# Optimization experiments

Measured on AMD Instinct MI355X. Metric: run time of the kernel, lower is better.

The kernel has to match this reference:

```python
import jax, jax.numpy as jnp
import numpy as np

N_NODES = 100000
N_EDGES = 3200000
N_FEAT = 128
DIM = 64
N_GRAPHS = 4096
EPS = 1e-5


def setup_inputs() -> dict:
    key = jax.random.key(0)
    ks = jax.random.split(key, 20)
    x = jax.random.normal(ks[0], (N_NODES, N_FEAT), dtype=jnp.float32)
    edge_index = jax.random.randint(ks[1], (2, N_EDGES), 0, N_NODES, dtype=jnp.int64)
    batch = jnp.sort(jax.random.randint(ks[2], (N_NODES,), 0, N_GRAPHS, dtype=jnp.int64))
    s = 0.1
    inp = {
        "x": x, "edge_index": edge_index, "batch": batch,
        "w1": jax.random.normal(ks[3], (N_FEAT, DIM), jnp.float32) * s,
        "b1": jnp.zeros((DIM,), jnp.float32),
        "bn1_g": 1.0 + s * jax.random.normal(ks[4], (DIM,), jnp.float32),
        "bn1_b": s * jax.random.normal(ks[5], (DIM,), jnp.float32),
        "conv_w": jax.random.normal(ks[6], (3, DIM, DIM), jnp.float32) * s,
        "conv_b": jnp.zeros((3, DIM), jnp.float32),
        "bnc_g": 1.0 + s * jax.random.normal(ks[7], (3, DIM), jnp.float32),
        "bnc_b": s * jax.random.normal(ks[8], (3, DIM), jnp.float32),
        "mlp_w": jax.random.normal(ks[9], (3, DIM, DIM), jnp.float32) * s,
        "mlp_b": jnp.zeros((3, DIM), jnp.float32),
        "bnm_g": 1.0 + s * jax.random.normal(ks[10], (3, DIM), jnp.float32),
        "bnm_b": s * jax.random.normal(ks[11], (3, DIM), jnp.float32),
        "out_w": jax.random.normal(ks[12], (DIM, 1), jnp.float32) * s,
        "out_b": jnp.zeros((1,), jnp.float32),
    }
    return inp


def _batchnorm(h, g, b):
    # training-mode BN: batch stats over the node/graph axis, biased variance
    m = jnp.mean(h, axis=0)
    v = jnp.var(h, axis=0)
    return (h - m) * jax.lax.rsqrt(v + EPS) * g + b


def _forward(x, edge_index, batch, w1, b1, bn1_g, bn1_b, conv_w, conv_b,
             bnc_g, bnc_b, mlp_w, mlp_b, bnm_g, bnm_b, out_w, out_b):
    src, dst = edge_index[0], edge_index[1]
    n = x.shape[0]
    # degree with self-loops (GCNConv default: add_self_loops=True, sym norm)
    deg = jax.ops.segment_sum(jnp.ones((src.shape[0],), x.dtype), dst, num_segments=n) + 1.0
    dis = jax.lax.rsqrt(deg)                  # D^{-1/2}
    enorm = (dis[src] * dis[dst])[:, None]    # per-edge norm [E,1]
    self_norm = (dis * dis)[:, None]          # self-loop norm = 1/deg [N,1]

    def gcn(h, W, b):
        h = h @ W                                                  # lin first (PyG)
        agg = jax.ops.segment_sum(h[src] * enorm, dst, num_segments=n)
        return agg + h * self_norm + b

    h = _batchnorm(jax.nn.relu(gcn(x, w1, b1)), bn1_g, bn1_b)
    for i in range(3):
        h = _batchnorm(gcn(h, conv_w[i], conv_b[i]), bnc_g[i], bnc_b[i])
    p = jax.ops.segment_sum(h, batch, num_segments=N_GRAPHS)       # global_add_pool
    for i in range(3):
        p = _batchnorm(jax.nn.relu(p @ mlp_w[i] + mlp_b[i]), bnm_g[i], bnm_b[i])
        # dropout: eval mode -> identity
    return p @ out_w + out_b


def reference(x, edge_index, batch, w1, b1, bn1_g, bn1_b, conv_w, conv_b,
              bnc_g, bnc_b, mlp_w, mlp_b, bnm_g, bnm_b, out_w, out_b):
    return _forward(x, edge_index, batch, w1, b1, bn1_g, bn1_b, conv_w, conv_b,
                    bnc_g, bnc_b, mlp_w, mlp_b, bnm_g, bnm_b, out_w, out_b)
```

## Files before the change

kernel.cpp:

```cpp
#include <hip/hip_runtime.h>
#include <hip/hip_bf16.h>

#define N_FEAT 128
#define DIM 64


__global__ void hist_kernel(const int* __restrict__ dst, int E, int* __restrict__ cnt) {
    int e = blockIdx.x * blockDim.x + threadIdx.x;
    if (e < E) atomicAdd(&cnt[dst[e]], 1);
}

__global__ void dis_kernel(const int* __restrict__ cnt, float* __restrict__ dis, int N) {
    int i = blockIdx.x * blockDim.x + threadIdx.x;
    if (i < N) dis[i] = rsqrtf((float)cnt[i] + 1.0f);
}

__global__ void scanA_kernel(const int* __restrict__ cnt, int N,
                             int* __restrict__ tmp, int* __restrict__ blk) {
    __shared__ int ts[256];
    int t = threadIdx.x;
    int base = blockIdx.x * 1024 + t * 4;
    int v[4];
    int s = 0;
#pragma unroll
    for (int j = 0; j < 4; j++) {
        int i = base + j;
        v[j] = (i < N) ? ((cnt[i] + 7) & ~7) : 0;
        s += v[j];
    }
    ts[t] = s;
    __syncthreads();
    for (int off = 1; off < 256; off <<= 1) {
        int x = (t >= off) ? ts[t - off] : 0;
        __syncthreads();
        ts[t] += x;
        __syncthreads();
    }
    int run = ts[t] - s;
#pragma unroll
    for (int j = 0; j < 4; j++) {
        run += v[j];
        int i = base + j;
        if (i < N) tmp[i] = run;
    }
    if (t == 255) blk[blockIdx.x] = ts[255];
}

__global__ void scanB_kernel(int* __restrict__ blk, int nb) {
    __shared__ int ts[128];
    int t = threadIdx.x;
    int v = (t < nb) ? blk[t] : 0;
    ts[t] = v;
    __syncthreads();
    for (int off = 1; off < 128; off <<= 1) {
        int x = (t >= off) ? ts[t - off] : 0;
        __syncthreads();
        ts[t] += x;
        __syncthreads();
    }
    if (t < nb) blk[t] = ts[t] - v;
}

__global__ void scanC_kernel(const int* __restrict__ tmp, const int* __restrict__ blk,
                             const int* __restrict__ cnt,
                             int N, int* __restrict__ rowp, int* __restrict__ cur) {
    int i = blockIdx.x * blockDim.x + threadIdx.x;
    if (i < N) {
        int b = i >> 10;
        int local = i & 1023;
        int excl = blk[b] + (local ? tmp[i - 1] : 0);
        rowp[i] = excl;
        cur[i] = excl;
        if (i == N - 1) rowp[N] = excl + ((cnt[i] + 7) & ~7);
    }
}

#define NSLICE 256
__global__ __launch_bounds__(256) void fill8_kernel(
    const int* __restrict__ src, const int* __restrict__ dst, int E,
    const float* __restrict__ dis, int* __restrict__ cur,
    int2* __restrict__ ecw, int npx ) {
    int xcd = blockIdx.x & 7;
    int slice = blockIdx.x >> 3;
    int per = (E + NSLICE - 1) / NSLICE;
    int lo = slice * per;
    int hi = min(lo + per, E);
    int dlo = xcd * npx, dhi = dlo + npx;
    for (int e = lo + threadIdx.x; e < hi; e += 256) {
        int d = dst[e];
        if (d >= dlo && d < dhi) {
            int s = src[e];
            int pos = atomicAdd(&cur[d], 1);
            ecw[pos] = make_int2(s << 8, __float_as_int(dis[s] * dis[d]));
        }
    }
}

__global__ void pad_kernel(const int* __restrict__ cur, const int* __restrict__ rowp,
                           int2* __restrict__ ecw, int N) {
    int i = blockIdx.x * blockDim.x + threadIdx.x;
    if (i < N) {
        int p = cur[i], e = rowp[i + 1];
        for (; p < e; p++) ecw[p] = make_int2(0, 0);
    }
}


template<int K, bool AFFINE, bool BIAS, bool RELU, bool STATS>
__global__ __launch_bounds__(256) void gemm_kernel(
    const float* __restrict__ A, const float* __restrict__ W,
    const float* __restrict__ scale, const float* __restrict__ shift,
    const float* __restrict__ bias, float* __restrict__ C,
    float* __restrict__ stats, int M)
{
    __shared__ float As[64][K + 4];
    __shared__ float Ws[K][64];
    __shared__ float bs[64], bq[64];
    int t = threadIdx.x;
    int row0 = blockIdx.x * 64;

    for (int q = t; q < K * 16; q += 256) {
        int k = q >> 4, c4 = (q & 15) << 2;
        float4 w = *reinterpret_cast<const float4*>(&W[k * 64 + c4]);
        *reinterpret_cast<float4*>(&Ws[k][c4]) = w;
    }
    for (int q = t; q < 64 * (K / 4); q += 256) {
        int r = q / (K / 4);
        int k4 = (q % (K / 4)) * 4;
        int row = row0 + r;
        float4 a;
        if (row < M) {
            a = *reinterpret_cast<const float4*>(&A[(size_t)row * K + k4]);
            if (AFFINE) {
                a.x = a.x * scale[k4]     + shift[k4];
                a.y = a.y * scale[k4 + 1] + shift[k4 + 1];
                a.z = a.z * scale[k4 + 2] + shift[k4 + 2];
                a.w = a.w * scale[k4 + 3] + shift[k4 + 3];
            }
        } else {
            a = make_float4(0.f, 0.f, 0.f, 0.f);
        }
        *reinterpret_cast<float4*>(&As[r][k4]) = a;
    }
    __syncthreads();

    int ty = t >> 4, tx = t & 15;
    int r0 = ty * 4, c0 = tx * 4;
    float acc[4][4] = {};
#pragma unroll 2
    for (int k = 0; k < K; k += 4) {
        float4 A0 = *reinterpret_cast<const float4*>(&As[r0 + 0][k]);
        float4 A1 = *reinterpret_cast<const float4*>(&As[r0 + 1][k]);
        float4 A2 = *reinterpret_cast<const float4*>(&As[r0 + 2][k]);
        float4 A3 = *reinterpret_cast<const float4*>(&As[r0 + 3][k]);
        float ar[4][4] = {{A0.x, A0.y, A0.z, A0.w}, {A1.x, A1.y, A1.z, A1.w},
                          {A2.x, A2.y, A2.z, A2.w}, {A3.x, A3.y, A3.z, A3.w}};
#pragma unroll
        for (int kk = 0; kk < 4; kk++) {
            float4 w = *reinterpret_cast<const float4*>(&Ws[k + kk][c0]);
#pragma unroll
            for (int i = 0; i < 4; i++) {
                acc[i][0] += ar[i][kk] * w.x;
                acc[i][1] += ar[i][kk] * w.y;
                acc[i][2] += ar[i][kk] * w.z;
                acc[i][3] += ar[i][kk] * w.w;
            }
        }
    }

    if (STATS) {
        if (t < 64) { bs[t] = 0.f; bq[t] = 0.f; }
        __syncthreads();
    }
    float ssum[4] = {0.f, 0.f, 0.f, 0.f}, ssq[4] = {0.f, 0.f, 0.f, 0.f};
#pragma unroll
    for (int i = 0; i < 4; i++) {
        int row = row0 + r0 + i;
        if (row < M) {
            float4 v;
            float* vp = &v.x;
#pragma unroll
            for (int j = 0; j < 4; j++) {
                float x = acc[i][j];
                if (BIAS) x += bias[c0 + j];
                if (RELU) x = fmaxf(x, 0.f);
                vp[j] = x;
                if (STATS) { ssum[j] += x; ssq[j] += x * x; }
            }
            *reinterpret_cast<float4*>(&C[(size_t)row * 64 + c0]) = v;
        }
    }
    if (STATS) {
#pragma unroll
        for (int j = 0; j < 4; j++) {
            atomicAdd(&bs[c0 + j], ssum[j]);
            atomicAdd(&bq[c0 + j], ssq[j]);
        }
        __syncthreads();
        if (t < 64) {
            atomicAdd(&stats[t], bs[t]);
            atomicAdd(&stats[64 + t], bq[t]);
        }
    }
}


#define LOADP(P, ebase)                                     \
    _Pragma("unroll") for (int j = 0; j < 4; j++)           \
        P[j] = ecw4[((ebase) >> 1) + j];

#define FMAG(P) {                                                          \
    float h[8];                                                            \
    _Pragma("unroll") for (int j = 0; j < 4; j++) {                        \
        h[2*j]   = *(const float*)(Hb + ((unsigned)P[j].x + lane4));       \
        h[2*j+1] = *(const float*)(Hb + ((unsigned)P[j].z + lane4));       \
    }                                                                      \
    _Pragma("unroll") for (int j = 0; j < 4; j++) {                        \
        acc += h[2*j]   * __int_as_float(P[j].y);                          \
        acc += h[2*j+1] * __int_as_float(P[j].w);                          \
    } }

template<bool RELU>
__global__ __launch_bounds__(256) void agg_kernel(
    const float* __restrict__ H, const int* __restrict__ rowp,
    const int2* __restrict__ ecw,
    const float* __restrict__ dis, const float* __restrict__ bias,
    float* __restrict__ Hout, float* __restrict__ stats, int N)
{
    __shared__ float bs[64], bq[64];
    const int4* ecw4 = (const int4*)ecw;
    int t = threadIdx.x;
    int lane = t & 63;
    unsigned lane4 = (unsigned)lane << 2;
    const char* Hb = (const char*)H;
    int base = (blockIdx.x * 4 + (t >> 6)) * 8;
    float b = bias[lane];
    float ssum = 0.f, ssq = 0.f;
    for (int u = 0; u < 8; u++) {
        int n = base + u;
        if (n >= N) break;
        int e0 = rowp[n], e1 = rowp[n + 1];
        float acc = 0.f;
        int ng = (e1 - e0) >> 3;
        if (ng > 0) {
            int4 pa[4], pb[4];
            int e = e0;
            LOADP(pa, e);
            int rem = ng - 1;
            while (rem >= 2) {
                LOADP(pb, e + 8); FMAG(pa);
                LOADP(pa, e + 16); FMAG(pb);
                e += 16; rem -= 2;
            }
            if (rem == 1) { LOADP(pb, e + 8); FMAG(pa); FMAG(pb); }
            else { FMAG(pa); }
        }
        float dn = dis[n];
        acc += H[(size_t)n * 64 + lane] * (dn * dn);
        acc += b;
        if (RELU) acc = fmaxf(acc, 0.f);
        Hout[(size_t)n * 64 + lane] = acc;
        ssum += acc;
        ssq += acc * acc;
    }
    if (t < 64) { bs[t] = 0.f; bq[t] = 0.f; }
    __syncthreads();
    atomicAdd(&bs[lane], ssum);
    atomicAdd(&bq[lane], ssq);
    __syncthreads();
    if (t < 64) {
        atomicAdd(&stats[t], bs[t]);
        atomicAdd(&stats[64 + t], bq[t]);
    }
}


__global__ void bnprep_kernel(const float* __restrict__ stats, const float* __restrict__ g,
                              const float* __restrict__ b, float* __restrict__ ss, float cntInv) {
    int c = threadIdx.x;
    float mean = stats[c] * cntInv;
    float var = stats[64 + c] * cntInv - mean * mean;
    float sc = g[c] * rsqrtf(var + 1e-5f);
    ss[c] = sc;
    ss[64 + c] = b[c] - mean * sc;
}


__global__ __launch_bounds__(256) void pool_kernel(
    const float* __restrict__ H, const int* __restrict__ batch,
    const float* __restrict__ ss, float* __restrict__ P, int N)
{
    int t = threadIdx.x;
    int lane = t & 63;
    int base = (blockIdx.x * 4 + (t >> 6)) * 8;
    float sc = ss[lane], sh = ss[64 + lane];
    float acc = 0.f;
    int gprev = -1;
    for (int u = 0; u < 8; u++) {
        int n = base + u;
        if (n >= N) break;
        int g = batch[n];
        if (g != gprev) {
            if (gprev >= 0) atomicAdd(&P[(size_t)gprev * 64 + lane], acc);
            acc = 0.f;
            gprev = g;
        }
        acc += H[(size_t)n * 64 + lane] * sc + sh;
    }
    if (gprev >= 0) atomicAdd(&P[(size_t)gprev * 64 + lane], acc);
}


__global__ __launch_bounds__(256) void final_kernel(
    const float* __restrict__ P, const float* __restrict__ ss,
    const float* __restrict__ outw, const float* __restrict__ outb,
    float* __restrict__ out, int G)
{
    int t = threadIdx.x;
    int lane = t & 63;
    int g = blockIdx.x * 4 + (t >> 6);
    if (g >= G) return;
    float v = (P[(size_t)g * 64 + lane] * ss[lane] + ss[64 + lane]) * outw[lane];
#pragma unroll
    for (int off = 32; off >= 1; off >>= 1) v += __shfl_xor(v, off, 64);
    if (lane == 0) out[g] = v + outb[0];
}


extern "C" void kernel_launch(void* const* d_in, const int* in_sizes, int n_in,
                              void* d_out, int out_size, void* d_ws, size_t ws_size,
                              hipStream_t stream)
{
    const float* x      = (const float*)d_in[0];
    const int*   ei     = (const int*)d_in[1];
    const int*   batch  = (const int*)d_in[2];
    const float* w1     = (const float*)d_in[3];
    const float* b1     = (const float*)d_in[4];
    const float* bn1_g  = (const float*)d_in[5];
    const float* bn1_b  = (const float*)d_in[6];
    const float* conv_w = (const float*)d_in[7];
    const float* conv_b = (const float*)d_in[8];
    const float* bnc_g  = (const float*)d_in[9];
    const float* bnc_b  = (const float*)d_in[10];
    const float* mlp_w  = (const float*)d_in[11];
    const float* mlp_b  = (const float*)d_in[12];
    const float* bnm_g  = (const float*)d_in[13];
    const float* bnm_b  = (const float*)d_in[14];
    const float* out_w  = (const float*)d_in[15];
    const float* out_b  = (const float*)d_in[16];
    float* out = (float*)d_out;

    const int N = in_sizes[0] / N_FEAT;
    const int E = in_sizes[1] / 2;
    const int G = out_size;
    const int* esrc = ei;
    const int* edst = ei + E;

    char* ws = (char*)d_ws;
    size_t off = 0;
    auto alloc = [&](size_t bytes) {
        size_t cur = off;
        off += (bytes + 255) & ~(size_t)255;
        return (void*)(ws + cur);
    };

    int*   deg   = (int*)alloc((size_t)N * 4);
    float* dis   = (float*)alloc((size_t)N * 4);
    int*   rtmp  = (int*)alloc((size_t)N * 4);
    int*   rowp  = (int*)alloc((size_t)(N + 1) * 4);
    int*   cur   = (int*)alloc((size_t)N * 4);
    int*   blk   = (int*)alloc(256 * 4);
    int2*  ecw   = (int2*)alloc(((size_t)E + 8ull * N) * 8);
    float* bufA  = (float*)alloc((size_t)(N + 64) * 64 * 4);
    float* bufB  = (float*)alloc((size_t)(N + 64) * 64 * 4);
    float* stats = (float*)alloc(7 * 128 * 4);
    float* ssbuf = (float*)alloc(7 * 128 * 4);
    float* P     = (float*)alloc((size_t)G * 64 * 4);
    float* pA    = (float*)alloc((size_t)G * 64 * 4);
    float* pB    = (float*)alloc((size_t)G * 64 * 4);

    hipMemsetAsync(deg, 0, (size_t)N * 4, stream);
    hipMemsetAsync(stats, 0, 7 * 128 * 4, stream);
    hipMemsetAsync(P, 0, (size_t)G * 64 * 4, stream);

    hist_kernel<<<(E + 255) / 256, 256, 0, stream>>>(edst, E, deg);
    dis_kernel<<<(N + 255) / 256, 256, 0, stream>>>(deg, dis, N);
    int nchunk = (N + 1023) / 1024;
    scanA_kernel<<<nchunk, 256, 0, stream>>>(deg, N, rtmp, blk);
    scanB_kernel<<<1, 128, 0, stream>>>(blk, nchunk);
    scanC_kernel<<<(N + 255) / 256, 256, 0, stream>>>(rtmp, blk, deg, N, rowp, cur);
    int npx = (N + 7) / 8;
    fill8_kernel<<<NSLICE * 8, 256, 0, stream>>>(esrc, edst, E, dis, cur, ecw, npx);
    pad_kernel<<<(N + 255) / 256, 256, 0, stream>>>(cur, rowp, ecw, N);

    int gemmN_grid = (N + 63) / 64;
    int aggN_grid = (N + 31) / 32;

    gemm_kernel<128, false, false, false, false><<<gemmN_grid, 256, 0, stream>>>(
        x, w1, nullptr, nullptr, nullptr, bufA, nullptr, N);
    agg_kernel<true><<<aggN_grid, 256, 0, stream>>>(
        bufA, rowp, ecw, dis, b1, bufB, stats, N);
    bnprep_kernel<<<1, 64, 0, stream>>>(stats, bn1_g, bn1_b, ssbuf, 1.0f / N);

    for (int i = 0; i < 3; i++) {
        const float* W  = conv_w + (size_t)i * 64 * 64;
        const float* bb = conv_b + (size_t)i * 64;
        float* st     = stats + (size_t)(1 + i) * 128;
        float* ss_in  = ssbuf + (size_t)i * 128;
        float* ss_out = ssbuf + (size_t)(1 + i) * 128;
        gemm_kernel<64, true, false, false, false><<<gemmN_grid, 256, 0, stream>>>(
            bufB, W, ss_in, ss_in + 64, nullptr, bufA, nullptr, N);
        agg_kernel<false><<<aggN_grid, 256, 0, stream>>>(
            bufA, rowp, ecw, dis, bb, bufB, st, N);
        bnprep_kernel<<<1, 64, 0, stream>>>(st, bnc_g + (size_t)i * 64, bnc_b + (size_t)i * 64,
                                            ss_out, 1.0f / N);
    }

    pool_kernel<<<aggN_grid, 256, 0, stream>>>(bufB, batch, ssbuf + 3 * 128, P, N);

    int gemmG_grid = (G + 63) / 64;
    gemm_kernel<64, false, true, true, true><<<gemmG_grid, 256, 0, stream>>>(
        P, mlp_w, nullptr, nullptr, mlp_b, pA, stats + 4 * 128, G);
    bnprep_kernel<<<1, 64, 0, stream>>>(stats + 4 * 128, bnm_g, bnm_b, ssbuf + 4 * 128, 1.0f / G);

    gemm_kernel<64, true, true, true, true><<<gemmG_grid, 256, 0, stream>>>(
        pA, mlp_w + 64 * 64, ssbuf + 4 * 128, ssbuf + 4 * 128 + 64,
        mlp_b + 64, pB, stats + 5 * 128, G);
    bnprep_kernel<<<1, 64, 0, stream>>>(stats + 5 * 128, bnm_g + 64, bnm_b + 64, ssbuf + 5 * 128, 1.0f / G);

    gemm_kernel<64, true, true, true, true><<<gemmG_grid, 256, 0, stream>>>(
        pB, mlp_w + 2 * 64 * 64, ssbuf + 5 * 128, ssbuf + 5 * 128 + 64,
        mlp_b + 2 * 64, pA, stats + 6 * 128, G);
    bnprep_kernel<<<1, 64, 0, stream>>>(stats + 6 * 128, bnm_g + 2 * 64, bnm_b + 2 * 64, ssbuf + 6 * 128, 1.0f / G);

    final_kernel<<<(G + 3) / 4, 256, 0, stream>>>(pA, ssbuf + 6 * 128, out_w, out_b, out, G);
}
```

Measured before the change: 1.131 ms.

## Factor symmetric GCN norm into GEMM row scaling and shrink edge records

```diff
diff --git a/kernel.cpp b/kernel.cpp
--- a/kernel.cpp
+++ b/kernel.cpp
@@ -7,7 +7,7 @@
 
 __global__ void hist_kernel(const int* __restrict__ dst, int E, int* __restrict__ cnt) {
     int e = blockIdx.x * blockDim.x + threadIdx.x;
-    if (e < E) atomicAdd(&cnt[dst[e]], 1);
+    if (e < E) atomicAdd(&cnt[__builtin_nontemporal_load(&dst[e])], 1);
 }
 
 __global__ void dis_kernel(const int* __restrict__ cnt, float* __restrict__ dis, int N) {
@@ -78,8 +78,7 @@
 #define NSLICE 256
 __global__ __launch_bounds__(256) void fill8_kernel(
     const int* __restrict__ src, const int* __restrict__ dst, int E,
-    const float* __restrict__ dis, int* __restrict__ cur,
-    int2* __restrict__ ecw, int npx ) {
+    int* __restrict__ cur, int* __restrict__ ecwi, int npx) {
     int xcd = blockIdx.x & 7;
     int slice = blockIdx.x >> 3;
     int per = (E + NSLICE - 1) / NSLICE;
@@ -87,31 +86,32 @@
     int hi = min(lo + per, E);
     int dlo = xcd * npx, dhi = dlo + npx;
     for (int e = lo + threadIdx.x; e < hi; e += 256) {
-        int d = dst[e];
+        int d = __builtin_nontemporal_load(&dst[e]);
         if (d >= dlo && d < dhi) {
-            int s = src[e];
+            int s = __builtin_nontemporal_load(&src[e]);
             int pos = atomicAdd(&cur[d], 1);
-            ecw[pos] = make_int2(s << 8, __float_as_int(dis[s] * dis[d]));
+            ecwi[pos] = s << 8;
         }
     }
 }
 
 __global__ void pad_kernel(const int* __restrict__ cur, const int* __restrict__ rowp,
-                           int2* __restrict__ ecw, int N) {
+                           int* __restrict__ ecwi, int N) {
     int i = blockIdx.x * blockDim.x + threadIdx.x;
     if (i < N) {
         int p = cur[i], e = rowp[i + 1];
-        for (; p < e; p++) ecw[p] = make_int2(0, 0);
-    }
-}
-
-
-template<int K, bool AFFINE, bool BIAS, bool RELU, bool STATS>
+        int dummy = N << 8;
+        for (; p < e; p++) ecwi[p] = dummy;
+    }
+}
+
+
+template<int K, bool AFFINE, bool BIAS, bool RELU, bool STATS, bool DISSCALE>
 __global__ __launch_bounds__(256) void gemm_kernel(
     const float* __restrict__ A, const float* __restrict__ W,
     const float* __restrict__ scale, const float* __restrict__ shift,
-    const float* __restrict__ bias, float* __restrict__ C,
-    float* __restrict__ stats, int M)
+    const float* __restrict__ bias, const float* __restrict__ dis,
+    float* __restrict__ C, float* __restrict__ stats, int M)
 {
     __shared__ float As[64][K + 4];
     __shared__ float Ws[K][64];
@@ -177,11 +177,13 @@
     for (int i = 0; i < 4; i++) {
         int row = row0 + r0 + i;
         if (row < M) {
+            float dsc = DISSCALE ? dis[row] : 1.f;
             float4 v;
             float* vp = &v.x;
 #pragma unroll
             for (int j = 0; j < 4; j++) {
                 float x = acc[i][j];
+                if (DISSCALE) x *= dsc;
                 if (BIAS) x += bias[c0 + j];
                 if (RELU) x = fmaxf(x, 0.f);
                 vp[j] = x;
@@ -205,30 +207,27 @@
 }
 
 
-#define LOADP(P, ebase)                                     \
-    _Pragma("unroll") for (int j = 0; j < 4; j++)           \
-        P[j] = ecw4[((ebase) >> 1) + j];
-
-#define FMAG(P) {                                                          \
-    float h[8];                                                            \
-    _Pragma("unroll") for (int j = 0; j < 4; j++) {                        \
-        h[2*j]   = *(const float*)(Hb + ((unsigned)P[j].x + lane4));       \
-        h[2*j+1] = *(const float*)(Hb + ((unsigned)P[j].z + lane4));       \
-    }                                                                      \
-    _Pragma("unroll") for (int j = 0; j < 4; j++) {                        \
-        acc += h[2*j]   * __int_as_float(P[j].y);                          \
-        acc += h[2*j+1] * __int_as_float(P[j].w);                          \
-    } }
+#define SUM8(Q0, Q1) {                                                     \
+    float h0 = *(const float*)(Hb + ((unsigned)Q0.x + lane4));             \
+    float h1 = *(const float*)(Hb + ((unsigned)Q0.y + lane4));             \
+    float h2 = *(const float*)(Hb + ((unsigned)Q0.z + lane4));             \
+    float h3 = *(const float*)(Hb + ((unsigned)Q0.w + lane4));             \
+    float h4 = *(const float*)(Hb + ((unsigned)Q1.x + lane4));             \
+    float h5 = *(const float*)(Hb + ((unsigned)Q1.y + lane4));             \
+    float h6 = *(const float*)(Hb + ((unsigned)Q1.z + lane4));             \
+    float h7 = *(const float*)(Hb + ((unsigned)Q1.w + lane4));             \
+    acc += ((h0 + h1) + (h2 + h3)) + ((h4 + h5) + (h6 + h7));              \
+}
 
 template<bool RELU>
 __global__ __launch_bounds__(256) void agg_kernel(
     const float* __restrict__ H, const int* __restrict__ rowp,
-    const int2* __restrict__ ecw,
+    const int* __restrict__ ecwi,
     const float* __restrict__ dis, const float* __restrict__ bias,
     float* __restrict__ Hout, float* __restrict__ stats, int N)
 {
     __shared__ float bs[64], bq[64];
-    const int4* ecw4 = (const int4*)ecw;
+    const int4* rec4 = (const int4*)ecwi;
     int t = threadIdx.x;
     int lane = t & 63;
     unsigned lane4 = (unsigned)lane << 2;
@@ -243,21 +242,26 @@
         float acc = 0.f;
         int ng = (e1 - e0) >> 3;
         if (ng > 0) {
-            int4 pa[4], pb[4];
-            int e = e0;
-            LOADP(pa, e);
+            int g4 = e0 >> 2;
+            int4 a0 = rec4[g4], a1 = rec4[g4 + 1];
             int rem = ng - 1;
             while (rem >= 2) {
-                LOADP(pb, e + 8); FMAG(pa);
-                LOADP(pa, e + 16); FMAG(pb);
-                e += 16; rem -= 2;
+                int4 b0 = rec4[g4 + 2], b1 = rec4[g4 + 3];
+                SUM8(a0, a1);
+                a0 = rec4[g4 + 4]; a1 = rec4[g4 + 5];
+                SUM8(b0, b1);
+                g4 += 4; rem -= 2;
             }
-            if (rem == 1) { LOADP(pb, e + 8); FMAG(pa); FMAG(pb); }
-            else { FMAG(pa); }
-        }
-        float dn = dis[n];
-        acc += H[(size_t)n * 64 + lane] * (dn * dn);
-        acc += b;
+            if (rem == 1) {
+                int4 b0 = rec4[g4 + 2], b1 = rec4[g4 + 3];
+                SUM8(a0, a1);
+                SUM8(b0, b1);
+            } else {
+                SUM8(a0, a1);
+            }
+        }
+        acc += H[(size_t)n * 64 + lane];
+        acc = acc * dis[n] + b;
         if (RELU) acc = fmaxf(acc, 0.f);
         Hout[(size_t)n * 64 + lane] = acc;
         ssum += acc;
@@ -370,7 +374,7 @@
     int*   rowp  = (int*)alloc((size_t)(N + 1) * 4);
     int*   cur   = (int*)alloc((size_t)N * 4);
     int*   blk   = (int*)alloc(256 * 4);
-    int2*  ecw   = (int2*)alloc(((size_t)E + 8ull * N) * 8);
+    int*   ecwi  = (int*)alloc(((size_t)E + 8ull * N) * 4);
     float* bufA  = (float*)alloc((size_t)(N + 64) * 64 * 4);
     float* bufB  = (float*)alloc((size_t)(N + 64) * 64 * 4);
     float* stats = (float*)alloc(7 * 128 * 4);
@@ -382,6 +386,7 @@
     hipMemsetAsync(deg, 0, (size_t)N * 4, stream);
     hipMemsetAsync(stats, 0, 7 * 128 * 4, stream);
     hipMemsetAsync(P, 0, (size_t)G * 64 * 4, stream);
+    hipMemsetAsync(bufA + (size_t)N * 64, 0, 64 * 4, stream);
 
     hist_kernel<<<(E + 255) / 256, 256, 0, stream>>>(edst, E, deg);
     dis_kernel<<<(N + 255) / 256, 256, 0, stream>>>(deg, dis, N);
@@ -390,16 +395,16 @@
     scanB_kernel<<<1, 128, 0, stream>>>(blk, nchunk);
     scanC_kernel<<<(N + 255) / 256, 256, 0, stream>>>(rtmp, blk, deg, N, rowp, cur);
     int npx = (N + 7) / 8;
-    fill8_kernel<<<NSLICE * 8, 256, 0, stream>>>(esrc, edst, E, dis, cur, ecw, npx);
-    pad_kernel<<<(N + 255) / 256, 256, 0, stream>>>(cur, rowp, ecw, N);
+    fill8_kernel<<<NSLICE * 8, 256, 0, stream>>>(esrc, edst, E, cur, ecwi, npx);
+    pad_kernel<<<(N + 255) / 256, 256, 0, stream>>>(cur, rowp, ecwi, N);
 
     int gemmN_grid = (N + 63) / 64;
     int aggN_grid = (N + 31) / 32;
 
-    gemm_kernel<128, false, false, false, false><<<gemmN_grid, 256, 0, stream>>>(
-        x, w1, nullptr, nullptr, nullptr, bufA, nullptr, N);
+    gemm_kernel<128, false, false, false, false, true><<<gemmN_grid, 256, 0, stream>>>(
+        x, w1, nullptr, nullptr, nullptr, dis, bufA, nullptr, N);
     agg_kernel<true><<<aggN_grid, 256, 0, stream>>>(
-        bufA, rowp, ecw, dis, b1, bufB, stats, N);
+        bufA, rowp, ecwi, dis, b1, bufB, stats, N);
     bnprep_kernel<<<1, 64, 0, stream>>>(stats, bn1_g, bn1_b, ssbuf, 1.0f / N);
 
     for (int i = 0; i < 3; i++) {
@@ -408,10 +413,10 @@
         float* st     = stats + (size_t)(1 + i) * 128;
         float* ss_in  = ssbuf + (size_t)i * 128;
         float* ss_out = ssbuf + (size_t)(1 + i) * 128;
-        gemm_kernel<64, true, false, false, false><<<gemmN_grid, 256, 0, stream>>>(
-            bufB, W, ss_in, ss_in + 64, nullptr, bufA, nullptr, N);
+        gemm_kernel<64, true, false, false, false, true><<<gemmN_grid, 256, 0, stream>>>(
+            bufB, W, ss_in, ss_in + 64, nullptr, dis, bufA, nullptr, N);
         agg_kernel<false><<<aggN_grid, 256, 0, stream>>>(
-            bufA, rowp, ecw, dis, bb, bufB, st, N);
+            bufA, rowp, ecwi, dis, bb, bufB, st, N);
         bnprep_kernel<<<1, 64, 0, stream>>>(st, bnc_g + (size_t)i * 64, bnc_b + (size_t)i * 64,
                                             ss_out, 1.0f / N);
     }
@@ -419,18 +424,18 @@
     pool_kernel<<<aggN_grid, 256, 0, stream>>>(bufB, batch, ssbuf + 3 * 128, P, N);
 
     int gemmG_grid = (G + 63) / 64;
-    gemm_kernel<64, false, true, true, true><<<gemmG_grid, 256, 0, stream>>>(
-        P, mlp_w, nullptr, nullptr, mlp_b, pA, stats + 4 * 128, G);
+    gemm_kernel<64, false, true, true, true, false><<<gemmG_grid, 256, 0, stream>>>(
+        P, mlp_w, nullptr, nullptr, mlp_b, nullptr, pA, stats + 4 * 128, G);
     bnprep_kernel<<<1, 64, 0, stream>>>(stats + 4 * 128, bnm_g, bnm_b, ssbuf + 4 * 128, 1.0f / G);
 
-    gemm_kernel<64, true, true, true, true><<<gemmG_grid, 256, 0, stream>>>(
+    gemm_kernel<64, true, true, true, true, false><<<gemmG_grid, 256, 0, stream>>>(
         pA, mlp_w + 64 * 64, ssbuf + 4 * 128, ssbuf + 4 * 128 + 64,
-        mlp_b + 64, pB, stats + 5 * 128, G);
+        mlp_b + 64, nullptr, pB, stats + 5 * 128, G);
     bnprep_kernel<<<1, 64, 0, stream>>>(stats + 5 * 128, bnm_g + 64, bnm_b + 64, ssbuf + 5 * 128, 1.0f / G);
 
-    gemm_kernel<64, true, true, true, true><<<gemmG_grid, 256, 0, stream>>>(
+    gemm_kernel<64, true, true, true, true, false><<<gemmG_grid, 256, 0, stream>>>(
         pB, mlp_w + 2 * 64 * 64, ssbuf + 5 * 128, ssbuf + 5 * 128 + 64,
-        mlp_b + 2 * 64, pA, stats + 6 * 128, G);
+        mlp_b + 2 * 64, nullptr, pA, stats + 6 * 128, G);
     bnprep_kernel<<<1, 64, 0, stream>>>(stats + 6 * 128, bnm_g + 2 * 64, bnm_b + 2 * 64, ssbuf + 6 * 128, 1.0f / G);
 
     final_kernel<<<(G + 3) / 4, 256, 0, stream>>>(pA, ssbuf + 6 * 128, out_w, out_b, out, G);
```

New measurement: 1.109 ms. No clear change (-2.0%).
